# Optimization experiments

Measured on AMD Instinct MI355X. Metric: run time of the kernel, lower is better.

Reference implementation:

```python
import jax, jax.numpy as jnp
import numpy as np

B, S, N, D, QD = 32, 256, 50, 100, 768


def _xavier(key, fan_out, fan_in):
    lim = float(np.sqrt(6.0 / (fan_in + fan_out)))
    return jax.random.uniform(key, (fan_out, fan_in), jnp.float32, -lim, lim)


def setup_inputs() -> dict:
    key = jax.random.key(0)
    ks = jax.random.split(key, 8)
    q = jax.random.normal(ks[0], (B, QD), jnp.float32)
    k = jax.random.normal(ks[1], (B, S, N, D), jnp.float32)
    v = jax.random.normal(ks[2], (B, S, N, D), jnp.float32)
    input_ent = jax.random.randint(ks[3], (B, S), 0, 100000)
    Q_w = _xavier(ks[4], D, QD)
    V_w = _xavier(ks[5], D, D)
    bq = 1.0 / np.sqrt(QD)
    bv = 1.0 / np.sqrt(D)
    Q_b = jax.random.uniform(ks[6], (D,), jnp.float32, -bq, bq)
    V_b = jax.random.uniform(ks[7], (D,), jnp.float32, -bv, bv)
    return {"input_ent": input_ent, "q": q, "k": k, "v": v,
            "Q_w": Q_w, "Q_b": Q_b, "V_w": V_w, "V_b": V_b}


def reference(input_ent, q, k, v, Q_w, Q_b, V_w, V_b):
    # Q projection + L2 normalize over feature dim (F.normalize eps=1e-12)
    Q = q @ Q_w.T + Q_b                                            # [B, D]
    Qn = Q / jnp.maximum(jnp.linalg.norm(Q, axis=1, keepdims=True), 1e-12)
    # Keys/values share the same V_linear projection of v (k arg unused, as in source)
    K = jnp.einsum('bsnd,ed->bsne', v, V_w) + V_b                  # [B, S, N, D]
    # detached L2 norm with zero->1e-6 replacement
    l2 = jax.lax.stop_gradient(jnp.linalg.norm(K, axis=3, keepdims=True))
    l2 = jnp.where(l2 == 0.0, 1e-6, l2)
    Kn = K / l2
    # cosine-similarity scores over neighbors
    att = jnp.einsum('bd,bsnd->bsn', Qn, Kn)                       # [B, S, N]
    att = jnp.where(att == 0.0, -10000.0, att)
    att = jax.nn.softmax(jax.nn.leaky_relu(att, 0.01), axis=2)
    # zero out positions where softmax was exactly uniform (pad rows)
    att = jnp.where(att == 1.0 / att.shape[-1], 0.0, att)
    # weighted sum of values (V_linear(v) == K)
    out = jnp.einsum('bsn,bsnd->bsd', att, K)                      # [B, S, D]
    # mode == 'candidate': return combined directly (graphsage=False)
    return out
```

## Files before the change

kernel.cpp:

```cpp
#include <hip/hip_runtime.h>
#include <math.h>


#define S_DIM 256
#define N_NBR 50
#define D_F   100
#define QD    768
#define NT    7
#define KC    4

typedef __attribute__((ext_vector_type(4))) float f32x4;
typedef __attribute__((ext_vector_type(8))) short s16x8;

__device__ __forceinline__ short f2bf(float f) {
  union { float f; unsigned u; } x; x.f = f;
  unsigned r = x.u + 0x7fffu + ((x.u >> 16) & 1u);
  return (short)(r >> 16);
}

__global__ __launch_bounds__(256, 2) void wga_kernel(
    const float* __restrict__ v, const float* __restrict__ q,
    const float* __restrict__ Qw, const float* __restrict__ Qb,
    const float* __restrict__ Vw, const float* __restrict__ Vb,
    float* __restrict__ out) {
  __shared__ __align__(16) short BlS[28 * 64 * 8];
  __shared__ float qs[QD];
  __shared__ float Qpart[256];
  __shared__ float QnS[112];
  __shared__ float rnS;
  __shared__ float nrm2W[4][64], srwW[4][64], attW[4][64];

  const int t  = threadIdx.x;
  const int w  = t >> 6, l = t & 63;
  const int qd = l >> 4, m = l & 15;
  const int blk = blockIdx.x;
  const int b   = blk >> 4;
  const int s0  = (blk & 15) << 4;

  for (int i = t; i < QD; i += 256) qs[i] = q[b * QD + i];

  for (int idx = t; idx < 28 * 64; idx += 256) {
    const int g  = idx >> 6, ll = idx & 63;
    const int c  = g / 7, nt = g - 7 * c;
    const int col = nt * 16 + (ll & 15);
    const int k0  = c * 32 + (ll >> 4) * 8;
    s16x8 pk;
    if (c < 3 && col < D_F) {
      const f32x4 u0 = *(const f32x4*)(Vw + col * D_F + k0);
      const f32x4 u1 = *(const f32x4*)(Vw + col * D_F + k0 + 4);
#pragma unroll
      for (int j = 0; j < 4; ++j) { pk[j] = f2bf(u0[j]); pk[4 + j] = f2bf(u1[j]); }
    } else {
#pragma unroll
      for (int j = 0; j < 8; ++j) {
        const int k = k0 + j;
        pk[j] = f2bf((col < D_F && k < D_F) ? Vw[col * D_F + k] : 0.f);
      }
    }
    *(s16x8*)&BlS[idx * 8] = pk;
  }
  __syncthreads();

  if (t < 200) {
    const int e = t >> 1, h = t & 1;
    const float4* wr = (const float4*)(Qw + e * QD + h * 384);
    const float4* qv = (const float4*)(qs + h * 384);
    float a0 = 0.f, a1 = 0.f, a2 = 0.f, a3 = 0.f;
#pragma unroll 4
    for (int f = 0; f < 96; ++f) {
      float4 wv = wr[f], qf = qv[f];
      a0 += wv.x * qf.x; a1 += wv.y * qf.y; a2 += wv.z * qf.z; a3 += wv.w * qf.w;
    }
    Qpart[t] = (a0 + a1) + (a2 + a3);
  }
  __syncthreads();
  if (t < D_F)       QnS[t] = Qpart[2 * t] + Qpart[2 * t + 1] + Qb[t];
  else if (t < 112)  QnS[t] = 0.f;
  __syncthreads();
  if (w == 0) {
    float x = QnS[l] * QnS[l];
    if (l < 48) x += QnS[64 + l] * QnS[64 + l];
#pragma unroll
    for (int d = 1; d < 64; d <<= 1) x += __shfl_xor(x, d, 64);
    if (l == 0) rnS = 1.0f / fmaxf(sqrtf(x), 1e-12f);
  }
  __syncthreads();
  if (t < D_F) QnS[t] *= rnS;
  __syncthreads();

  float QnSv[NT], bias[NT];
#pragma unroll
  for (int nt = 0; nt < NT; ++nt) {
    const int col = nt * 16 + m;
    QnSv[nt] = QnS[col];
    bias[nt] = (col < D_F) ? Vb[col] : 0.f;
  }

  for (int tt = 0; tt < 4; ++tt) {
    const int s = s0 + (tt << 2) + w;
    const float* vb = v + (size_t)(b * S_DIM + s) * (N_NBR * D_F);

    s16x8 afr[4][KC];
#pragma unroll
    for (int hp = 0; hp < 2; ++hp) {
      f32x4 L[2][KC], H[2][KC];
#pragma unroll
      for (int i = 0; i < 2; ++i) {
        const int mt  = hp * 2 + i;
        const int row = mt * 16 + m;
        const bool rv = row < N_NBR;
        const float* ap = vb + row * D_F;
#pragma unroll
        for (int c = 0; c < KC; ++c) {
          const int k0 = c * 32 + qd * 8;
          f32x4 z = {0.f, 0.f, 0.f, 0.f};
          L[i][c] = z; H[i][c] = z;
          if (rv && k0 <= 96) L[i][c] = *(const f32x4*)(ap + k0);
          if (rv && k0 <= 92) H[i][c] = *(const f32x4*)(ap + k0 + 4);
        }
      }
#pragma unroll
      for (int i = 0; i < 2; ++i)
#pragma unroll
        for (int c = 0; c < KC; ++c) {
          s16x8 pa;
#pragma unroll
          for (int j = 0; j < 4; ++j) { pa[j] = f2bf(L[i][c][j]); pa[4 + j] = f2bf(H[i][c][j]); }
          afr[hp * 2 + i][c] = pa;
        }
    }

    f32x4 acc[4][NT];
#pragma unroll
    for (int mt = 0; mt < 4; ++mt)
#pragma unroll
      for (int nt = 0; nt < NT; ++nt) {
        f32x4 bz; bz[0] = bias[nt]; bz[1] = bias[nt]; bz[2] = bias[nt]; bz[3] = bias[nt];
        acc[mt][nt] = bz;
      }
#pragma unroll
    for (int c = 0; c < KC; ++c) {
      s16x8 bf[NT];
#pragma unroll
      for (int nt = 0; nt < NT; ++nt)
        bf[nt] = *(const s16x8*)&BlS[(((c * 7 + nt) << 6) + l) * 8];
#pragma unroll
      for (int mt = 0; mt < 4; ++mt)
#pragma unroll
        for (int nt = 0; nt < NT; ++nt)
          acc[mt][nt] = __builtin_amdgcn_mfma_f32_16x16x32_bf16(afr[mt][c], bf[nt], acc[mt][nt], 0, 0, 0);
    }

#pragma unroll
    for (int mt = 0; mt < 4; ++mt)
#pragma unroll
      for (int r = 0; r < 4; ++r) {
        float np = 0.f, sp = 0.f;
#pragma unroll
        for (int nt = 0; nt < NT; ++nt) {
          const float kv = acc[mt][nt][r];
          np += kv * kv;
          sp += QnSv[nt] * kv;
        }
#pragma unroll
        for (int d = 1; d < 16; d <<= 1) {
          np += __shfl_xor(np, d, 64);
          sp += __shfl_xor(sp, d, 64);
        }
        if (m == 0) {
          const int row = mt * 16 + qd * 4 + r;
          nrm2W[w][row] = np; srwW[w][row] = sp;
        }
      }

    {
      float a = -1e30f;
      if (l < N_NBR) {
        float l2 = sqrtf(nrm2W[w][l]);
        if (l2 == 0.f) l2 = 1e-6f;
        float sc = srwW[w][l] / l2;
        if (sc == 0.f) sc = -10000.f;
        a = (sc >= 0.f) ? sc : 0.01f * sc;
      }
      float mx = a;
#pragma unroll
      for (int d = 1; d < 64; d <<= 1) mx = fmaxf(mx, __shfl_xor(mx, d, 64));
      const float e = (l < N_NBR) ? __expf(a - mx) : 0.f;
      float sm = e;
#pragma unroll
      for (int d = 1; d < 64; d <<= 1) sm += __shfl_xor(sm, d, 64);
      float att = e / sm;
      if (att == 0.02f) att = 0.f;
      attW[w][l] = (l < N_NBR) ? att : 0.f;
    }

    float ar[4][4];
#pragma unroll
    for (int mt = 0; mt < 4; ++mt)
#pragma unroll
      for (int r = 0; r < 4; ++r)
        ar[mt][r] = attW[w][mt * 16 + qd * 4 + r];

    float o[NT];
#pragma unroll
    for (int nt = 0; nt < NT; ++nt) {
      float ov = 0.f;
#pragma unroll
      for (int mt = 0; mt < 4; ++mt)
#pragma unroll
        for (int r = 0; r < 4; ++r)
          ov = fmaf(ar[mt][r], acc[mt][nt][r], ov);
      ov += __shfl_xor(ov, 16, 64);
      ov += __shfl_xor(ov, 32, 64);
      o[nt] = ov;
    }
    const float slo = (qd == 0) ? o[0] : (qd == 1) ? o[1] : (qd == 2) ? o[2] : o[3];
    const float shi = (qd == 0) ? o[4] : (qd == 1) ? o[5] : o[6];
    float* op = out + (size_t)(b * S_DIM + s) * D_F;
    op[l] = slo;
    if (l < 36) op[64 + l] = shi;
  }
}

extern "C" void kernel_launch(void* const* d_in, const int* in_sizes, int n_in,
                              void* d_out, int out_size, void* d_ws, size_t ws_size,
                              hipStream_t stream) {
  const float* q  = (const float*)d_in[1];
  const float* v  = (const float*)d_in[3];
  const float* Qw = (const float*)d_in[4];
  const float* Qb = (const float*)d_in[5];
  const float* Vw = (const float*)d_in[6];
  const float* Vb = (const float*)d_in[7];
  float* out = (float*)d_out;
  (void)d_ws; (void)ws_size;

  wga_kernel<<<512, 256, 0, stream>>>(v, q, Qw, Qb, Vw, Vb, out);
}
```

Before: 398.6 us.

## Software-pipeline A-fragment loads one K-chunk ahead of MFMA compute

Replaces the bulk load of all A fragments per s-row with a register double-buffer. The next K-chunk, or the first chunk of the next s-row, is prefetched while the current chunk is converted to bf16 and fed to MFMA, so global load latency overlaps with matrix work. This lowers register pressure by not holding all 16 fragments at once. The risk is that the non-unrolled loops (unroll 1) add loop overhead and restrict how the compiler schedules instructions.

```diff
diff --git a/kernel.cpp b/kernel.cpp
--- a/kernel.cpp
+++ b/kernel.cpp
@@ -96,40 +96,27 @@
     bias[nt] = (col < D_F) ? Vb[col] : 0.f;
   }
 
+  f32x4 Lb[4], Hb[4];
+  auto loadA = [&](int tti, int c) {
+    const int ss = s0 + (tti << 2) + w;
+    const float* vbp = v + (size_t)(b * S_DIM + ss) * (N_NBR * D_F);
+    const int k0 = c * 32 + qd * 8;
+#pragma unroll
+    for (int mt = 0; mt < 4; ++mt) {
+      const int row = mt * 16 + m;
+      const bool rv = row < N_NBR;
+      const float* ap = vbp + row * D_F + k0;
+      f32x4 z = {0.f, 0.f, 0.f, 0.f};
+      Lb[mt] = z; Hb[mt] = z;
+      if (rv && k0 <= 96) Lb[mt] = *(const f32x4*)(ap);
+      if (rv && k0 <= 92) Hb[mt] = *(const f32x4*)(ap + 4);
+    }
+  };
+
+  loadA(0, 0);
+
+#pragma unroll 1
   for (int tt = 0; tt < 4; ++tt) {
-    const int s = s0 + (tt << 2) + w;
-    const float* vb = v + (size_t)(b * S_DIM + s) * (N_NBR * D_F);
-
-    s16x8 afr[4][KC];
-#pragma unroll
-    for (int hp = 0; hp < 2; ++hp) {
-      f32x4 L[2][KC], H[2][KC];
-#pragma unroll
-      for (int i = 0; i < 2; ++i) {
-        const int mt  = hp * 2 + i;
-        const int row = mt * 16 + m;
-        const bool rv = row < N_NBR;
-        const float* ap = vb + row * D_F;
-#pragma unroll
-        for (int c = 0; c < KC; ++c) {
-          const int k0 = c * 32 + qd * 8;
-          f32x4 z = {0.f, 0.f, 0.f, 0.f};
-          L[i][c] = z; H[i][c] = z;
-          if (rv && k0 <= 96) L[i][c] = *(const f32x4*)(ap + k0);
-          if (rv && k0 <= 92) H[i][c] = *(const f32x4*)(ap + k0 + 4);
-        }
-      }
-#pragma unroll
-      for (int i = 0; i < 2; ++i)
-#pragma unroll
-        for (int c = 0; c < KC; ++c) {
-          s16x8 pa;
-#pragma unroll
-          for (int j = 0; j < 4; ++j) { pa[j] = f2bf(L[i][c][j]); pa[4 + j] = f2bf(H[i][c][j]); }
-          afr[hp * 2 + i][c] = pa;
-        }
-    }
-
     f32x4 acc[4][NT];
 #pragma unroll
     for (int mt = 0; mt < 4; ++mt)
@@ -138,8 +125,20 @@
         f32x4 bz; bz[0] = bias[nt]; bz[1] = bias[nt]; bz[2] = bias[nt]; bz[3] = bias[nt];
         acc[mt][nt] = bz;
       }
-#pragma unroll
+
+#pragma unroll 1
     for (int c = 0; c < KC; ++c) {
+      s16x8 pa[4];
+#pragma unroll
+      for (int mt = 0; mt < 4; ++mt) {
+        s16x8 p;
+#pragma unroll
+        for (int j = 0; j < 4; ++j) { p[j] = f2bf(Lb[mt][j]); p[4 + j] = f2bf(Hb[mt][j]); }
+        pa[mt] = p;
+      }
+      if (c < KC - 1)      loadA(tt, c + 1);
+      else if (tt < 3)     loadA(tt + 1, 0);
+
       s16x8 bf[NT];
 #pragma unroll
       for (int nt = 0; nt < NT; ++nt)
@@ -148,7 +147,7 @@
       for (int mt = 0; mt < 4; ++mt)
 #pragma unroll
         for (int nt = 0; nt < NT; ++nt)
-          acc[mt][nt] = __builtin_amdgcn_mfma_f32_16x16x32_bf16(afr[mt][c], bf[nt], acc[mt][nt], 0, 0, 0);
+          acc[mt][nt] = __builtin_amdgcn_mfma_f32_16x16x32_bf16(pa[mt], bf[nt], acc[mt][nt], 0, 0, 0);
     }
 
 #pragma unroll
@@ -214,6 +213,7 @@
       ov += __shfl_xor(ov, 32, 64);
       o[nt] = ov;
     }
+    const int s = s0 + (tt << 2) + w;
     const float slo = (qd == 0) ? o[0] : (qd == 1) ? o[1] : (qd == 2) ? o[2] : o[3];
     const float shi = (qd == 0) ? o[4] : (qd == 1) ? o[5] : o[6];
     float* op = out + (size_t)(b * S_DIM + s) * D_F;
```

Result: faster. 349.1 us (-12.4%).
